# Kernel tuning notes

Hardware: AMD Instinct MI355X
Metric: run time of the kernel (lower is better)

The kernel has to match this reference:

```python
import jax, jax.numpy as jnp
import numpy as np

T = 2048   # block_size
V = 1024   # vocab_size
B = 8


def setup_inputs() -> dict:
    key = jax.random.key(0)
    k_idx, k_v = jax.random.split(key)
    idx = jax.random.randint(k_idx, (B, T), 0, V, dtype=jnp.int64 if jax.config.jax_enable_x64 else jnp.int32)
    # nn.Embedding(4,1) init: normal(mean=0, std=0.02) (the constant init is overwritten)
    v_weight = jax.random.normal(k_v, (4, 1), dtype=jnp.float32) * 0.02
    return {"idx": idx, "v_weight": v_weight}


def reference(idx, v_weight):
    # one-hot token 'embedding': [B, T, V]
    e = jax.nn.one_hot(idx, V, dtype=jnp.float32)

    # relative position table: pos[i,j] = i-j, clamped: <0 -> 3 (padding), >2 -> 2
    r = jnp.arange(T)
    d = r[:, None] - r[None, :]
    pidx = jnp.where(d < 0, 3, jnp.minimum(d, 2))            # [T, T] int

    tril = jnp.tril(jnp.ones((T, T), dtype=jnp.float32))     # lower-triangular mask

    # pos_embd = v(pos).squeeze().tril()
    pos_embd = v_weight[pidx, 0] * tril                      # [T, T]

    # layer_one = pos_embd @ e  -> [B, T, V]
    layer_one = jnp.einsum('ts,bsv->btv', pos_embd, e)

    # attention = e @ layer_one^T -> [B, T, T], then tril mask
    attention = jnp.einsum('btv,bsv->bts', e, layer_one)
    masked_attention = attention * tril                      # broadcast over batch

    # output = masked_attention @ e -> [B, T, V]
    logits = jnp.einsum('bts,bsv->btv', masked_attention, e)

    return jax.nn.softmax(logits, axis=-1)
```

## Files before the change

### kernel.cpp

```cpp
#include <hip/hip_runtime.h>

#define TT   2048
#define VV   1024
#define BB   8
#define ROCC 32

#define SEGP_OFF 0x000000
#define OCC_OFF  0x110000

__global__ __launch_bounds__(1024) void k_pre(const int* __restrict__ idx,
                                              float* __restrict__ SEGP,
                                              int* __restrict__ OCC) {
    __shared__ unsigned h[16][VV];
    const int b = blockIdx.x, tid = threadIdx.x;
    #pragma unroll
    for (int gp = 0; gp < 16; ++gp) h[gp][tid] = 0u;
    __syncthreads();

    const int tok0 = idx[b * TT + tid];
    const int tok1 = idx[b * TT + 1024 + tid];
    const int s0 = tid >> 6;
    const unsigned inc = 1u << ((s0 & 1) * 16);
    atomicAdd(&h[s0 >> 1][tok0], inc);
    atomicAdd(&h[8 + (s0 >> 1)][tok1], inc);
    __syncthreads();

    float* __restrict__ dst = SEGP + (size_t)b * 33 * VV + tid;
    unsigned run = 0;
    #pragma unroll
    for (int gp = 0; gp < 16; ++gp) {
        const unsigned w = h[gp][tid];
        const unsigned b0 = run; run += (w & 0xffffu);
        const unsigned b1 = run; run += (w >> 16);
        h[gp][tid] = b0 | (b1 << 16);
        dst[(2 * gp)     * VV] = (float)b0;
        dst[(2 * gp + 1) * VV] = (float)b1;
    }
    dst[32 * VV] = (float)run;
    __syncthreads();

    const int lane = tid & 63;
    const unsigned long long lt = (lane == 0) ? 0ull : ((~0ull) >> (64 - lane));
    #pragma unroll
    for (int half = 0; half < 2; ++half) {
        const int seg = (tid >> 6) + half * 16;
        const int tok = half ? tok1 : tok0;
        unsigned long long mm = ~0ull;
        #pragma unroll
        for (int bit = 0; bit < 10; ++bit) {
            const unsigned long long bl = __ballot((tok >> bit) & 1);
            mm &= ((tok >> bit) & 1) ? bl : ~bl;
        }
        const int cnt = __popcll(mm & lt);
        const int base = (int)((h[seg >> 1][tok] >> ((seg & 1) * 16)) & 0xffffu);
        const int r0 = base + cnt;
        if (r0 < ROCC) OCC[((size_t)b * VV + tok) * ROCC + r0] = seg * 64 + lane;
    }
}

__global__ __launch_bounds__(64) void k_main(const int* __restrict__ idx,
                                             const float* __restrict__ wt,
                                             const float* __restrict__ SEGP,
                                             const int* __restrict__ OCC,
                                             float* __restrict__ out) {
    __shared__ __align__(16) float slabM[VV];
    __shared__ __align__(16) float slabN[VV];
    __shared__ __align__(16) float slabB[VV];
    const int lane = threadIdx.x;
    const int bc = blockIdx.x;
    const int b = bc >> 10, c = bc & (VV - 1);

    const float* __restrict__ segp_b = SEGP + (size_t)b * 33 * VV;
    int m = (int)segp_b[32 * VV + c];
    if (m == 0) return;
    if (m > ROCC) m = ROCC;
    const int* __restrict__ occ = OCC + ((size_t)b * VV + c) * ROCC;
    const int* __restrict__ row = idx + b * TT;
    const float w2 = wt[2], dw0 = wt[0] - w2, dw1 = wt[1] - w2;
    const int myocc = (lane < m) ? occ[lane] : 0;

    const float4 z = {0.0f, 0.0f, 0.0f, 0.0f};
    ((float4*)slabM)[lane] = z; ((float4*)slabM)[lane +  64] = z;
    ((float4*)slabM)[lane + 128] = z; ((float4*)slabM)[lane + 192] = z;
    ((float4*)slabB)[lane] = z; ((float4*)slabB)[lane +  64] = z;
    ((float4*)slabB)[lane + 128] = z; ((float4*)slabB)[lane + 192] = z;

    const int cq = c >> 6, cl = c & 63;
    float accM[16];
    #pragma unroll
    for (int q = 0; q < 16; ++q) accM[q] = 0.0f;
    float Kf = 0.0f;

    for (int K = 1; K <= m; ++K) {
        const int t = __shfl(myocc, K - 1, 64);
        const int p = t - 1;
        ((float4*)slabN)[lane] = z; ((float4*)slabN)[lane +  64] = z;
        ((float4*)slabN)[lane + 128] = z; ((float4*)slabN)[lane + 192] = z;

        float pr[16];
        int tok = 0, r = 63, g = 0;
        const bool have = (p >= 0);
        if (have) {
            g = p >> 6; r = p & 63;
            const int gd = (r < 32) ? g : g + 1;
            const float* __restrict__ prow = segp_b + (size_t)gd * VV;
            #pragma unroll
            for (int q = 0; q < 16; ++q) pr[q] = prow[q * 64 + lane];
            tok = row[(g << 6) + lane];
        } else {
            #pragma unroll
            for (int q = 0; q < 16; ++q) pr[q] = 0.0f;
        }
        Kf += 1.0f;

        asm volatile("s_waitcnt lgkmcnt(0)" ::: "memory");
        if (have) {
            if (r < 32) { if (lane <= r) atomicAdd(&slabN[tok],  1.0f); }
            else        { if (lane >  r) atomicAdd(&slabN[tok], -1.0f); }
        }
        asm volatile("s_waitcnt lgkmcnt(0)" ::: "memory");

        float acc[16];
        #pragma unroll
        for (int q = 0; q < 16; ++q) {
            const float sn  = slabN[q * 64 + lane];
            const float smv = slabM[q * 64 + lane] + sn;
            const float bg  = slabB[q * 64 + lane];
            slabM[q * 64 + lane] = smv;
            accM[q] += pr[q];
            const float Nv = pr[q] + sn;
            float a = w2 * (Kf * Nv - (accM[q] + smv)) + dw1 * bg;
            if (q == cq) a += (lane == cl) ? (w2 + dw0) * Kf : 0.0f;
            acc[q] = a;
        }
        if (K < m) {
            const int xn = row[t + 1];
            if (lane == 0) atomicAdd(&slabB[xn], 1.0f);
        }

        float mx = -1e30f;
        #pragma unroll
        for (int q = 0; q < 16; ++q) mx = fmaxf(mx, acc[q]);
        #pragma unroll
        for (int o = 32; o > 0; o >>= 1) mx = fmaxf(mx, __shfl_xor(mx, o, 64));
        float sm = 0.0f;
        #pragma unroll
        for (int q = 0; q < 16; ++q) { acc[q] = __expf(acc[q] - mx); sm += acc[q]; }
        #pragma unroll
        for (int o = 32; o > 0; o >>= 1) sm += __shfl_xor(sm, o, 64);
        const float inv = 1.0f / sm;

        float* __restrict__ op = out + (((size_t)b * TT + t) << 10);
        #pragma unroll
        for (int q = 0; q < 16; ++q)
            __builtin_nontemporal_store(acc[q] * inv, &op[q * 64 + lane]);
    }
}

extern "C" void kernel_launch(void* const* d_in, const int* in_sizes, int n_in,
                              void* d_out, int out_size, void* d_ws, size_t ws_size,
                              hipStream_t stream) {
    const int*   idx = (const int*)d_in[0];
    const float* w   = (const float*)d_in[1];
    float*       out = (float*)d_out;
    char* ws = (char*)d_ws;
    float* SEGP = (float*)(ws + SEGP_OFF);
    int*   OCC  = (int*)(ws + OCC_OFF);

    k_pre <<<BB,      1024, 0, stream>>>(idx, SEGP, OCC);
    k_main<<<BB * VV, 64,   0, stream>>>(idx, w, SEGP, OCC, out);
}
```

Measured before the change: 97.44 us.

## Pack slab accumulators into one shared array with encoded counts

Replaces the three shared slabs (M, N, B) with a single slab that packs the B counter in the low part and a scaled M-style term in multiples of 64. Per-iteration zeroing of slabN goes away, along with its separate read-modify-write. The algebra is rearranged so the N contribution is applied as a deferred atomic on the next iteration. This cuts LDS traffic and one barrier-like wait per iteration, in exchange for floor/fma decoding and float-precision risk if the encoded values grow large.

```diff
diff --git a/kernel.cpp b/kernel.cpp
--- a/kernel.cpp
+++ b/kernel.cpp
@@ -63,9 +63,7 @@
                                              const float* __restrict__ SEGP,
                                              const int* __restrict__ OCC,
                                              float* __restrict__ out) {
-    __shared__ __align__(16) float slabM[VV];
-    __shared__ __align__(16) float slabN[VV];
-    __shared__ __align__(16) float slabB[VV];
+    __shared__ __align__(16) float slab[VV];
     const int lane = threadIdx.x;
     const int bc = blockIdx.x;
     const int b = bc >> 10, c = bc & (VV - 1);
@@ -80,62 +78,62 @@
     const int myocc = (lane < m) ? occ[lane] : 0;
 
     const float4 z = {0.0f, 0.0f, 0.0f, 0.0f};
-    ((float4*)slabM)[lane] = z; ((float4*)slabM)[lane +  64] = z;
-    ((float4*)slabM)[lane + 128] = z; ((float4*)slabM)[lane + 192] = z;
-    ((float4*)slabB)[lane] = z; ((float4*)slabB)[lane +  64] = z;
-    ((float4*)slabB)[lane + 128] = z; ((float4*)slabB)[lane + 192] = z;
+    ((float4*)slab)[lane] = z; ((float4*)slab)[lane +  64] = z;
+    ((float4*)slab)[lane + 128] = z; ((float4*)slab)[lane + 192] = z;
 
     const int cq = c >> 6, cl = c & 63;
     float accM[16];
     #pragma unroll
     for (int q = 0; q < 16; ++q) accM[q] = 0.0f;
-    float Kf = 0.0f;
+
+    float pendv = 0.0f;
+    int   pendtok = 0;
+    bool  pend = false;
 
     for (int K = 1; K <= m; ++K) {
+        const float Kf = (float)K;
         const int t = __shfl(myocc, K - 1, 64);
         const int p = t - 1;
-        ((float4*)slabN)[lane] = z; ((float4*)slabN)[lane +  64] = z;
-        ((float4*)slabN)[lane + 128] = z; ((float4*)slabN)[lane + 192] = z;
 
         float pr[16];
-        int tok = 0, r = 63, g = 0;
+        int tok = 0;
+        float sgn = 0.0f;
         const bool have = (p >= 0);
         if (have) {
-            g = p >> 6; r = p & 63;
+            const int g = p >> 6, r = p & 63;
             const int gd = (r < 32) ? g : g + 1;
             const float* __restrict__ prow = segp_b + (size_t)gd * VV;
             #pragma unroll
             for (int q = 0; q < 16; ++q) pr[q] = prow[q * 64 + lane];
             tok = row[(g << 6) + lane];
+            sgn = (r < 32) ? ((lane <= r) ? 1.0f : 0.0f)
+                           : ((lane >  r) ? -1.0f : 0.0f);
         } else {
             #pragma unroll
             for (int q = 0; q < 16; ++q) pr[q] = 0.0f;
         }
-        Kf += 1.0f;
 
-        asm volatile("s_waitcnt lgkmcnt(0)" ::: "memory");
-        if (have) {
-            if (r < 32) { if (lane <= r) atomicAdd(&slabN[tok],  1.0f); }
-            else        { if (lane >  r) atomicAdd(&slabN[tok], -1.0f); }
-        }
+        if (pend)                         atomicAdd(&slab[pendtok], pendv);
+        if (have && K > 1 && sgn != 0.0f) atomicAdd(&slab[tok], 64.0f * (Kf - 1.0f) * sgn);
         asm volatile("s_waitcnt lgkmcnt(0)" ::: "memory");
 
         float acc[16];
         #pragma unroll
         for (int q = 0; q < 16; ++q) {
-            const float sn  = slabN[q * 64 + lane];
-            const float smv = slabM[q * 64 + lane] + sn;
-            const float bg  = slabB[q * 64 + lane];
-            slabM[q * 64 + lane] = smv;
+            const float val = slab[q * 64 + lane];
+            const float s  = floorf(val * 0.015625f);
+            const float bg = __builtin_fmaf(-64.0f, s, val);
             accM[q] += pr[q];
-            const float Nv = pr[q] + sn;
-            float a = w2 * (Kf * Nv - (accM[q] + smv)) + dw1 * bg;
+            float a = w2 * (Kf * pr[q] - accM[q] + s) + dw1 * bg;
             if (q == cq) a += (lane == cl) ? (w2 + dw0) * Kf : 0.0f;
             acc[q] = a;
         }
+        pend = (have && sgn != 0.0f);
+        pendtok = tok;
+        pendv = -64.0f * Kf * sgn;
         if (K < m) {
             const int xn = row[t + 1];
-            if (lane == 0) atomicAdd(&slabB[xn], 1.0f);
+            if (lane == 0) atomicAdd(&slab[xn], 1.0f);
         }
 
         float mx = -1e30f;
```

Result: faster. 92.13 us (-5.4%).
